# Performance work log

Hardware: AMD Instinct MI355X
Metric: run time of the kernel (lower is better)

The kernel has to match this reference:

```python
import jax, jax.numpy as jnp
import numpy as np

B, NK, NQ, DK, DQ, H, DV = 16, 256, 256, 256, 256, 128, 256
MASK_VAL = -1000000.0

def setup_inputs() -> dict:
    key = jax.random.key(0)
    ks = jax.random.split(key, 7)
    return {
        "key": jax.random.normal(ks[0], (B, NK, DK), dtype=jnp.float32),
        "query": jax.random.normal(ks[1], (B, NQ, DQ), dtype=jnp.float32),
        "value": jax.random.normal(ks[2], (B, NQ, DV), dtype=jnp.float32),
        "valid_lens": jax.random.randint(ks[3], (B,), 1, NQ + 1, dtype=jnp.int32),
        "Wk": jax.random.normal(ks[4], (DK, H), dtype=jnp.float32) / np.sqrt(DK),
        "Wq": jax.random.normal(ks[5], (DQ, H), dtype=jnp.float32) / np.sqrt(DQ),
        "wv": jax.random.normal(ks[6], (H,), dtype=jnp.float32) / np.sqrt(H),
    }

def reference(key, query, value, valid_lens, Wk, Wq, wv):
    k = key @ Wk                      # (B, NK, H)
    q = query @ Wq                    # (B, NQ, H)
    # note: original unsqueezes key at dim 2, query at dim 1 -> (B, NK, NQ, H)
    feature = jnp.tanh(k[:, :, None, :] + q[:, None, :, :])
    scores = jnp.einsum('bkqh,h->bkq', feature, wv)   # (B, NK, NQ)
    # mask along last (query) axis per batch, as repeat_interleave does
    pos = jnp.arange(scores.shape[-1])[None, None, :]
    masked = jnp.where(pos < valid_lens[:, None, None], scores, MASK_VAL)
    attn = jax.nn.softmax(masked, axis=-1)            # (B, NK, NQ)
    return jnp.einsum('bkq,bqd->bkd', attn, value)    # (B, NK, DV)
```

## Files before the change

### kernel.cpp

```cpp
#include <hip/hip_runtime.h>

#define B_   16
#define NK_  256
#define NQ_  256
#define DK_  256
#define H_   128
#define DV_  256

#define C2X 2.8853900817779268f
#define L2E 1.4426950408889634f
#define MASKV -1.0e5f

typedef float f4 __attribute__((ext_vector_type(4)));

__device__ __forceinline__ float exp2_fast(float x) { return __builtin_amdgcn_exp2f(x); }
__device__ __forceinline__ float rcp_fast(float x)  { return __builtin_amdgcn_rcpf(x); }

__global__ __launch_bounds__(256) void proj_kernel(
    const float* __restrict__ key, const float* __restrict__ query,
    const float* __restrict__ Wk,  const float* __restrict__ Wq,
    float* __restrict__ kfE, float* __restrict__ qE4)
{
    __shared__ alignas(16) float A_s[16 * 256];
    __shared__ alignas(16) float W_s[2][32 * 128];

    const int blk = blockIdx.x;
    const int tid = threadIdx.x;
    const bool isQ = blk >= 256;
    const int rb = (blk & 255) * 16;

    const float* __restrict__ A = isQ ? query : key;
    const float* __restrict__ W = isQ ? Wq : Wk;

    {
        const f4* src = (const f4*)(A + (size_t)rb * DK_);
        f4* dst = (f4*)A_s;
#pragma unroll
        for (int j = 0; j < 4; ++j) dst[tid + 256 * j] = src[tid + 256 * j];
    }
    f4 wr0, wr1, wr2, wr3;
    {
        const f4* ws = (const f4*)W;
        wr0 = ws[tid]; wr1 = ws[tid + 256]; wr2 = ws[tid + 512]; wr3 = ws[tid + 768];
    }

    const int rg2 = (tid >> 5) << 1;
    const int c4  = (tid & 31) << 2;

    f4 acc0 = {0.f, 0.f, 0.f, 0.f}, acc1 = acc0;

    for (int c = 0; c < 8; ++c) {
        {
            f4* wd = (f4*)&W_s[c & 1][0];
            wd[tid] = wr0; wd[tid + 256] = wr1; wd[tid + 512] = wr2; wd[tid + 768] = wr3;
        }
        __syncthreads();
        if (c < 7) {
            const f4* ws = (const f4*)(W + (size_t)(c + 1) * 32 * H_);
            wr0 = ws[tid]; wr1 = ws[tid + 256]; wr2 = ws[tid + 512]; wr3 = ws[tid + 768];
        }
        const float* Wb = &W_s[c & 1][0];
        const float* Ab = A_s + (c << 5);
#pragma unroll
        for (int k = 0; k < 32; k += 4) {
            f4 w0 = *(const f4*)(Wb + (k + 0) * H_ + c4);
            f4 w1 = *(const f4*)(Wb + (k + 1) * H_ + c4);
            f4 w2 = *(const f4*)(Wb + (k + 2) * H_ + c4);
            f4 w3 = *(const f4*)(Wb + (k + 3) * H_ + c4);
            f4 a0 = *(const f4*)(Ab + (rg2 + 0) * 256 + k);
            f4 a1 = *(const f4*)(Ab + (rg2 + 1) * 256 + k);
            acc0 += a0[0] * w0; acc1 += a1[0] * w0;
            acc0 += a0[1] * w1; acc1 += a1[1] * w1;
            acc0 += a0[2] * w2; acc1 += a1[2] * w2;
            acc0 += a0[3] * w3; acc1 += a1[3] * w3;
        }
    }

    f4 e0, e1;
#pragma unroll
    for (int cc = 0; cc < 4; ++cc) {
        e0[cc] = exp2_fast(C2X * acc0[cc]);
        e1[cc] = exp2_fast(C2X * acc1[cc]);
    }

    if (!isQ) {
        float* dst = kfE + (size_t)(rb + rg2) * H_ + c4;
        *(f4*)(dst)      = e0;
        *(f4*)(dst + H_) = e1;
    } else {
        const int b  = rb >> 8;
        const int q0 = (rb & 255) + rg2;
        f4* dst = (f4*)qE4 + ((size_t)(b * 32 + (c4 >> 2))) * NQ_ + q0;
        dst[0] = e0;
        dst[1] = e1;
    }
}

__global__ __launch_bounds__(512, 4) void attn_kernel(
    const float* __restrict__ kfE, const float* __restrict__ qE4,
    const float* __restrict__ value, const int* __restrict__ vlens,
    const float* __restrict__ wv, float* __restrict__ out)
{
    __shared__ alignas(16) float at_s[256 * 8];
    __shared__ alignas(16) float scratch[8192];

    const int x    = blockIdx.x;
    const int g    = x >> 4;
    const int b    = ((x & 15) + ((x >> 8) << 3)) & 15;
    const int k0   = g << 3;
    const int tid  = threadIdx.x;
    const int lane = tid & 63;
    const int wu   = __builtin_amdgcn_readfirstlane(tid >> 6);
    const int valid  = vlens[b];
    const int nchunk = (valid + 63) >> 6;

    float sumwv;
    {
        f4 sw = {0.f, 0.f, 0.f, 0.f};
#pragma unroll
        for (int i = 0; i < 32; ++i) sw += ((const f4*)wv)[i];
        sumwv = (sw[0] + sw[1]) + (sw[2] + sw[3]);
    }

    float* sc_s = scratch;

    {
        const int c  = wu >> 1;
        const int rh = wu & 1;
        if (c < nchunk) {
            const float* ekb = kfE + ((size_t)(b * NK_ + k0 + rh * 4)) * H_;
            const f4*    eqp = (const f4*)qE4 + ((size_t)b << 13) + (c << 6) + lane;
            const f4*    wvf = (const f4*)wv;

            float acc[4][2];
#pragma unroll
            for (int r = 0; r < 4; ++r) { acc[r][0] = 0.f; acc[r][1] = 0.f; }

#pragma unroll 4
            for (int h4 = 0; h4 < 32; ++h4) {
                const f4 e  = eqp[h4 << 8];
                const f4 w4 = wvf[h4];
#pragma unroll
                for (int r = 0; r < 4; ++r) {
                    const f4 ek = *(const f4*)(ekb + r * H_ + (h4 << 2));
                    acc[r][0] = fmaf(w4[0], rcp_fast(fmaf(ek[0], e[0], 1.f)), acc[r][0]);
                    acc[r][1] = fmaf(w4[1], rcp_fast(fmaf(ek[1], e[1], 1.f)), acc[r][1]);
                    acc[r][0] = fmaf(w4[2], rcp_fast(fmaf(ek[2], e[2], 1.f)), acc[r][0]);
                    acc[r][1] = fmaf(w4[3], rcp_fast(fmaf(ek[3], e[3], 1.f)), acc[r][1]);
                }
            }
            const int q = (c << 6) + lane;
#pragma unroll
            for (int r = 0; r < 4; ++r)
                sc_s[(rh * 4 + r) * 260 + q] = sumwv - 2.f * (acc[r][0] + acc[r][1]);
        }
    }
    __syncthreads();

    {
        const float* row = sc_s + wu * 260;
        float s[4];
        float m = MASKV;
#pragma unroll
        for (int j = 0; j < 4; ++j) {
            const int q = (j << 6) + lane;
            s[j] = (q < valid) ? row[q] : MASKV;
            m = fmaxf(m, s[j]);
        }
#pragma unroll
        for (int off = 32; off >= 1; off >>= 1)
            m = fmaxf(m, __shfl_xor(m, off, 64));
        float ssum = 0.f;
#pragma unroll
        for (int j = 0; j < 4; ++j) {
            s[j] = exp2_fast(L2E * (s[j] - m));
            ssum += s[j];
        }
#pragma unroll
        for (int off = 32; off >= 1; off >>= 1)
            ssum += __shfl_xor(ssum, off, 64);
        const float inv = rcp_fast(ssum);
#pragma unroll
        for (int j = 0; j < 4; ++j)
            at_s[(((j << 6) + lane) << 3) + wu] = s[j] * inv;
    }
    __syncthreads();

    float* red = scratch;
    {
        const int d4 = lane << 2;
        const float* vb = value + (size_t)b * (NQ_ * DV_) + d4;
        f4 o[8];
#pragma unroll
        for (int k = 0; k < 8; ++k) o[k] = (f4){0.f, 0.f, 0.f, 0.f};
#pragma unroll 4
        for (int q = wu; q < valid; q += 8) {
            const f4 v   = *(const f4*)(vb + (size_t)q * DV_);
            const f4 alo = *(const f4*)(at_s + (q << 3));
            const f4 ahi = *(const f4*)(at_s + (q << 3) + 4);
            o[0] += alo[0] * v; o[1] += alo[1] * v;
            o[2] += alo[2] * v; o[3] += alo[3] * v;
            o[4] += ahi[0] * v; o[5] += ahi[1] * v;
            o[6] += ahi[2] * v; o[7] += ahi[3] * v;
        }
        if (wu < 4) {
            float* rp = red + (wu << 11) + d4;
#pragma unroll
            for (int k = 0; k < 8; ++k) *(f4*)(rp + (k << 8)) = o[k];
        }
    }
    __syncthreads();
    {
        const int d4 = lane << 2;
        if (wu >= 4) {
            float* rp = red + ((wu - 4) << 11) + d4;
        }
    }
    {
        const int d4 = lane << 2;
    }
    __syncthreads();
    {
        const int d4 = lane << 2;
        const float* rp = red + (wu << 8) + d4;
        f4 oo = *(const f4*)(rp)        + *(const f4*)(rp + 2048)
              + *(const f4*)(rp + 4096) + *(const f4*)(rp + 6144);
        *(f4*)(out + ((size_t)(b * NK_ + k0 + wu)) * DV_ + d4) = oo;
    }
}

__global__ __launch_bounds__(512, 4) void attn_kernel2(
    const float* __restrict__ kfE, const float* __restrict__ qE4,
    const float* __restrict__ value, const int* __restrict__ vlens,
    const float* __restrict__ wv, float* __restrict__ out)
{
    __shared__ alignas(16) float at_s[256 * 8];
    __shared__ alignas(16) float scratch[8192];

    const int x    = blockIdx.x;
    const int g    = x >> 4;
    const int b    = ((x & 15) + ((x >> 8) << 3)) & 15;
    const int k0   = g << 3;
    const int tid  = threadIdx.x;
    const int lane = tid & 63;
    const int wu   = __builtin_amdgcn_readfirstlane(tid >> 6);
    const int valid  = vlens[b];
    const int nchunk = (valid + 63) >> 6;

    float sumwv;
    {
        f4 sw = {0.f, 0.f, 0.f, 0.f};
#pragma unroll
        for (int i = 0; i < 32; ++i) sw += ((const f4*)wv)[i];
        sumwv = (sw[0] + sw[1]) + (sw[2] + sw[3]);
    }

    float* sc_s = scratch;

    {
        const int c  = wu >> 1;
        const int rh = wu & 1;
        if (c < nchunk) {
            const float* ekb = kfE + ((size_t)(b * NK_ + k0 + rh * 4)) * H_;
            const f4*    eqp = (const f4*)qE4 + ((size_t)b << 13) + (c << 6) + lane;
            const f4*    wvf = (const f4*)wv;
            float acc[4][2];
#pragma unroll
            for (int r = 0; r < 4; ++r) { acc[r][0] = 0.f; acc[r][1] = 0.f; }
#pragma unroll 4
            for (int h4 = 0; h4 < 32; ++h4) {
                const f4 e  = eqp[h4 << 8];
                const f4 w4 = wvf[h4];
#pragma unroll
                for (int r = 0; r < 4; ++r) {
                    const f4 ek = *(const f4*)(ekb + r * H_ + (h4 << 2));
                    acc[r][0] = fmaf(w4[0], rcp_fast(fmaf(ek[0], e[0], 1.f)), acc[r][0]);
                    acc[r][1] = fmaf(w4[1], rcp_fast(fmaf(ek[1], e[1], 1.f)), acc[r][1]);
                    acc[r][0] = fmaf(w4[2], rcp_fast(fmaf(ek[2], e[2], 1.f)), acc[r][0]);
                    acc[r][1] = fmaf(w4[3], rcp_fast(fmaf(ek[3], e[3], 1.f)), acc[r][1]);
                }
            }
            const int q = (c << 6) + lane;
#pragma unroll
            for (int r = 0; r < 4; ++r)
                sc_s[(rh * 4 + r) * 260 + q] = sumwv - 2.f * (acc[r][0] + acc[r][1]);
        }
    }
    __syncthreads();

    {
        const float* row = sc_s + wu * 260;
        float s[4];
        float m = MASKV;
#pragma unroll
        for (int j = 0; j < 4; ++j) {
            const int q = (j << 6) + lane;
            s[j] = (q < valid) ? row[q] : MASKV;
            m = fmaxf(m, s[j]);
        }
#pragma unroll
        for (int off = 32; off >= 1; off >>= 1)
            m = fmaxf(m, __shfl_xor(m, off, 64));
        float ssum = 0.f;
#pragma unroll
        for (int j = 0; j < 4; ++j) {
            s[j] = exp2_fast(L2E * (s[j] - m));
            ssum += s[j];
        }
#pragma unroll
        for (int off = 32; off >= 1; off >>= 1)
            ssum += __shfl_xor(ssum, off, 64);
        const float inv = rcp_fast(ssum);
#pragma unroll
        for (int j = 0; j < 4; ++j)
            at_s[(((j << 6) + lane) << 3) + wu] = s[j] * inv;
    }
    __syncthreads();

    float* red = scratch;
    {
        const int d4 = lane << 2;
        const float* vb = value + (size_t)b * (NQ_ * DV_) + d4;
        f4 o[8];
#pragma unroll
        for (int k = 0; k < 8; ++k) o[k] = (f4){0.f, 0.f, 0.f, 0.f};
#pragma unroll 4
        for (int q = wu; q < valid; q += 8) {
            const f4 v   = *(const f4*)(vb + (size_t)q * DV_);
            const f4 alo = *(const f4*)(at_s + (q << 3));
            const f4 ahi = *(const f4*)(at_s + (q << 3) + 4);
            o[0] += alo[0] * v; o[1] += alo[1] * v;
            o[2] += alo[2] * v; o[3] += alo[3] * v;
            o[4] += ahi[0] * v; o[5] += ahi[1] * v;
            o[6] += ahi[2] * v; o[7] += ahi[3] * v;
        }
        if (wu < 4) {
            float* rp = red + (wu << 11) + d4;
#pragma unroll
            for (int k = 0; k < 8; ++k) *(f4*)(rp + (k << 8)) = o[k];
        }
        __syncthreads();
        if (wu >= 4) {
            float* rp = red + ((wu - 4) << 11) + d4;
#pragma unroll
            for (int k = 0; k < 8; ++k) {
                f4* p = (f4*)(rp + (k << 8));
                *p += o[k];
            }
        }
        __syncthreads();
        const float* rp = red + (wu << 8) + d4;
        f4 oo = *(const f4*)(rp)        + *(const f4*)(rp + 2048)
              + *(const f4*)(rp + 4096) + *(const f4*)(rp + 6144);
        *(f4*)(out + ((size_t)(b * NK_ + k0 + wu)) * DV_ + d4) = oo;
    }
}

extern "C" void kernel_launch(void* const* d_in, const int* in_sizes, int n_in,
                              void* d_out, int out_size, void* d_ws, size_t ws_size,
                              hipStream_t stream)
{
    const float* key   = (const float*)d_in[0];
    const float* query = (const float*)d_in[1];
    const float* value = (const float*)d_in[2];
    const int*   vlens = (const int*)  d_in[3];
    const float* Wk    = (const float*)d_in[4];
    const float* Wq    = (const float*)d_in[5];
    const float* wv    = (const float*)d_in[6];
    float* outp = (float*)d_out;

    float* kfE = (float*)d_ws;
    float* qE4 = kfE + (size_t)B_ * NK_ * H_;

    hipLaunchKernelGGL(proj_kernel, dim3(512), dim3(256), 0, stream,
                       key, query, Wk, Wq, kfE, qE4);
    hipLaunchKernelGGL(attn_kernel2, dim3(512), dim3(512), 0, stream,
                       kfE, qE4, value, vlens, wv, outp);
}
```

Measured before the change: 103.0 us.

## Use split-bf16 MFMA for projection GEMM and drop dead attention kernel

The projection kernel now uses bf16 MFMA matrix instructions with a hi/lo split (three MFMAs per tile) to keep close-to-fp32 accuracy, in place of scalar FMA. Each block covers 32 rows, so the grid is halved, and weights are converted straight from global memory into registers. The unused old attn_kernel is removed and attn_kernel2 is renamed to attn_kernel. Risks are the conversion overhead, the strided weight loads, and scalar scattered stores to the qE4 layout.

```diff
diff --git a/kernel.cpp b/kernel.cpp
--- a/kernel.cpp
+++ b/kernel.cpp
@@ -12,224 +12,125 @@
 #define MASKV -1.0e5f
 
 typedef float f4 __attribute__((ext_vector_type(4)));
+typedef short s4v    __attribute__((ext_vector_type(4)));
+typedef short bf16x8 __attribute__((ext_vector_type(8)));
 
 __device__ __forceinline__ float exp2_fast(float x) { return __builtin_amdgcn_exp2f(x); }
 __device__ __forceinline__ float rcp_fast(float x)  { return __builtin_amdgcn_rcpf(x); }
+
+__device__ __forceinline__ unsigned bf16_rne(float x) {
+    unsigned u = __builtin_bit_cast(unsigned, x);
+    return (u + 0x7FFFu + ((u >> 16) & 1u)) >> 16;
+}
+__device__ __forceinline__ float bf16_to_f(unsigned h) {
+    return __builtin_bit_cast(float, h << 16);
+}
 
 __global__ __launch_bounds__(256) void proj_kernel(
     const float* __restrict__ key, const float* __restrict__ query,
     const float* __restrict__ Wk,  const float* __restrict__ Wq,
     float* __restrict__ kfE, float* __restrict__ qE4)
 {
-    __shared__ alignas(16) float A_s[16 * 256];
-    __shared__ alignas(16) float W_s[2][32 * 128];
+    __shared__ alignas(16) short Ah_s[32 * 264];
+    __shared__ alignas(16) short Al_s[32 * 264];
 
     const int blk = blockIdx.x;
     const int tid = threadIdx.x;
-    const bool isQ = blk >= 256;
-    const int rb = (blk & 255) * 16;
-
-    const float* __restrict__ A = isQ ? query : key;
-    const float* __restrict__ W = isQ ? Wq : Wk;
-
-    {
-        const f4* src = (const f4*)(A + (size_t)rb * DK_);
-        f4* dst = (f4*)A_s;
-#pragma unroll
-        for (int j = 0; j < 4; ++j) dst[tid + 256 * j] = src[tid + 256 * j];
-    }
-    f4 wr0, wr1, wr2, wr3;
-    {
-        const f4* ws = (const f4*)W;
-        wr0 = ws[tid]; wr1 = ws[tid + 256]; wr2 = ws[tid + 512]; wr3 = ws[tid + 768];
-    }
-
-    const int rg2 = (tid >> 5) << 1;
-    const int c4  = (tid & 31) << 2;
-
-    f4 acc0 = {0.f, 0.f, 0.f, 0.f}, acc1 = acc0;
-
-    for (int c = 0; c < 8; ++c) {
-        {
-            f4* wd = (f4*)&W_s[c & 1][0];
-            wd[tid] = wr0; wd[tid + 256] = wr1; wd[tid + 512] = wr2; wd[tid + 768] = wr3;
-        }
-        __syncthreads();
-        if (c < 7) {
-            const f4* ws = (const f4*)(W + (size_t)(c + 1) * 32 * H_);
-            wr0 = ws[tid]; wr1 = ws[tid + 256]; wr2 = ws[tid + 512]; wr3 = ws[tid + 768];
-        }
-        const float* Wb = &W_s[c & 1][0];
-        const float* Ab = A_s + (c << 5);
-#pragma unroll
-        for (int k = 0; k < 32; k += 4) {
-            f4 w0 = *(const f4*)(Wb + (k + 0) * H_ + c4);
-            f4 w1 = *(const f4*)(Wb + (k + 1) * H_ + c4);
-            f4 w2 = *(const f4*)(Wb + (k + 2) * H_ + c4);
-            f4 w3 = *(const f4*)(Wb + (k + 3) * H_ + c4);
-            f4 a0 = *(const f4*)(Ab + (rg2 + 0) * 256 + k);
-            f4 a1 = *(const f4*)(Ab + (rg2 + 1) * 256 + k);
-            acc0 += a0[0] * w0; acc1 += a1[0] * w0;
-            acc0 += a0[1] * w1; acc1 += a1[1] * w1;
-            acc0 += a0[2] * w2; acc1 += a1[2] * w2;
-            acc0 += a0[3] * w3; acc1 += a1[3] * w3;
-        }
-    }
-
-    f4 e0, e1;
-#pragma unroll
-    for (int cc = 0; cc < 4; ++cc) {
-        e0[cc] = exp2_fast(C2X * acc0[cc]);
-        e1[cc] = exp2_fast(C2X * acc1[cc]);
-    }
-
-    if (!isQ) {
-        float* dst = kfE + (size_t)(rb + rg2) * H_ + c4;
-        *(f4*)(dst)      = e0;
-        *(f4*)(dst + H_) = e1;
-    } else {
-        const int b  = rb >> 8;
-        const int q0 = (rb & 255) + rg2;
-        f4* dst = (f4*)qE4 + ((size_t)(b * 32 + (c4 >> 2))) * NQ_ + q0;
-        dst[0] = e0;
-        dst[1] = e1;
-    }
+    const bool isQ = blk >= 128;
+    const int mbase = (blk & 127) << 5;
+
+    const float* __restrict__ Ag = isQ ? query : key;
+    const float* __restrict__ Wg = isQ ? Wq : Wk;
+
+    {
+        const int r  = tid >> 3;
+        const int kc = (tid & 7) << 5;
+        const f4* src = (const f4*)(Ag + (size_t)(mbase + r) * DK_ + kc);
+        s4v* dh = (s4v*)(Ah_s + r * 264 + kc);
+        s4v* dl = (s4v*)(Al_s + r * 264 + kc);
+#pragma unroll
+        for (int i = 0; i < 8; ++i) {
+            f4 v = src[i];
+            s4v h, l;
+#pragma unroll
+            for (int c = 0; c < 4; ++c) {
+                unsigned hb = bf16_rne(v[c]);
+                h[c] = (short)hb;
+                l[c] = (short)bf16_rne(v[c] - bf16_to_f(hb));
+            }
+            dh[i] = h;
+            dl[i] = l;
+        }
+    }
+    __syncthreads();
+
+    const int w  = tid >> 6;
+    const int l  = tid & 63;
+    const int lg = l >> 4;
+    const int ln = l & 15;
+
+    f4 acc[2][2] = {};
+
+#pragma unroll
+    for (int ks = 0; ks < 8; ++ks) {
+        const int k0 = ks << 5;
+
+        bf16x8 bh[2], bl[2];
+#pragma unroll
+        for (int nt = 0; nt < 2; ++nt) {
+            const float* bp = Wg + (size_t)(k0 + (lg << 3)) * H_
+                              + (w << 5) + (nt << 4) + ln;
+            float bv[8];
+#pragma unroll
+            for (int j = 0; j < 8; ++j) bv[j] = bp[(size_t)j * H_];
+#pragma unroll
+            for (int j = 0; j < 8; ++j) {
+                unsigned hb = bf16_rne(bv[j]);
+                bh[nt][j] = (short)hb;
+                bl[nt][j] = (short)bf16_rne(bv[j] - bf16_to_f(hb));
+            }
+        }
+
+        bf16x8 ah[2], al[2];
+#pragma unroll
+        for (int mt = 0; mt < 2; ++mt) {
+            const int m = (mt << 4) + ln;
+            ah[mt] = *(const bf16x8*)(Ah_s + m * 264 + k0 + (lg << 3));
+            al[mt] = *(const bf16x8*)(Al_s + m * 264 + k0 + (lg << 3));
+        }
+
+#pragma unroll
+        for (int mt = 0; mt < 2; ++mt)
+#pragma unroll
+            for (int nt = 0; nt < 2; ++nt) {
+                acc[mt][nt] = __builtin_amdgcn_mfma_f32_16x16x32_bf16(
+                    ah[mt], bh[nt], acc[mt][nt], 0, 0, 0);
+                acc[mt][nt] = __builtin_amdgcn_mfma_f32_16x16x32_bf16(
+                    al[mt], bh[nt], acc[mt][nt], 0, 0, 0);
+                acc[mt][nt] = __builtin_amdgcn_mfma_f32_16x16x32_bf16(
+                    ah[mt], bl[nt], acc[mt][nt], 0, 0, 0);
+            }
+    }
+
+#pragma unroll
+    for (int mt = 0; mt < 2; ++mt)
+#pragma unroll
+        for (int nt = 0; nt < 2; ++nt)
+#pragma unroll
+            for (int r = 0; r < 4; ++r) {
+                const float e = exp2_fast(C2X * acc[mt][nt][r]);
+                const int R = mbase + (mt << 4) + (lg << 2) + r;
+                const int h = (w << 5) + (nt << 4) + ln;
+                if (!isQ) {
+                    kfE[(size_t)R * H_ + h] = e;
+                } else {
+                    const int b = R >> 8, q = R & 255;
+                    qE4[(((size_t)(b * 32 + (h >> 2))) * NQ_ + q) * 4 + (h & 3)] = e;
+                }
+            }
 }
 
 __global__ __launch_bounds__(512, 4) void attn_kernel(
-    const float* __restrict__ kfE, const float* __restrict__ qE4,
-    const float* __restrict__ value, const int* __restrict__ vlens,
-    const float* __restrict__ wv, float* __restrict__ out)
-{
-    __shared__ alignas(16) float at_s[256 * 8];
-    __shared__ alignas(16) float scratch[8192];
-
-    const int x    = blockIdx.x;
-    const int g    = x >> 4;
-    const int b    = ((x & 15) + ((x >> 8) << 3)) & 15;
-    const int k0   = g << 3;
-    const int tid  = threadIdx.x;
-    const int lane = tid & 63;
-    const int wu   = __builtin_amdgcn_readfirstlane(tid >> 6);
-    const int valid  = vlens[b];
-    const int nchunk = (valid + 63) >> 6;
-
-    float sumwv;
-    {
-        f4 sw = {0.f, 0.f, 0.f, 0.f};
-#pragma unroll
-        for (int i = 0; i < 32; ++i) sw += ((const f4*)wv)[i];
-        sumwv = (sw[0] + sw[1]) + (sw[2] + sw[3]);
-    }
-
-    float* sc_s = scratch;
-
-    {
-        const int c  = wu >> 1;
-        const int rh = wu & 1;
-        if (c < nchunk) {
-            const float* ekb = kfE + ((size_t)(b * NK_ + k0 + rh * 4)) * H_;
-            const f4*    eqp = (const f4*)qE4 + ((size_t)b << 13) + (c << 6) + lane;
-            const f4*    wvf = (const f4*)wv;
-
-            float acc[4][2];
-#pragma unroll
-            for (int r = 0; r < 4; ++r) { acc[r][0] = 0.f; acc[r][1] = 0.f; }
-
-#pragma unroll 4
-            for (int h4 = 0; h4 < 32; ++h4) {
-                const f4 e  = eqp[h4 << 8];
-                const f4 w4 = wvf[h4];
-#pragma unroll
-                for (int r = 0; r < 4; ++r) {
-                    const f4 ek = *(const f4*)(ekb + r * H_ + (h4 << 2));
-                    acc[r][0] = fmaf(w4[0], rcp_fast(fmaf(ek[0], e[0], 1.f)), acc[r][0]);
-                    acc[r][1] = fmaf(w4[1], rcp_fast(fmaf(ek[1], e[1], 1.f)), acc[r][1]);
-                    acc[r][0] = fmaf(w4[2], rcp_fast(fmaf(ek[2], e[2], 1.f)), acc[r][0]);
-                    acc[r][1] = fmaf(w4[3], rcp_fast(fmaf(ek[3], e[3], 1.f)), acc[r][1]);
-                }
-            }
-            const int q = (c << 6) + lane;
-#pragma unroll
-            for (int r = 0; r < 4; ++r)
-                sc_s[(rh * 4 + r) * 260 + q] = sumwv - 2.f * (acc[r][0] + acc[r][1]);
-        }
-    }
-    __syncthreads();
-
-    {
-        const float* row = sc_s + wu * 260;
-        float s[4];
-        float m = MASKV;
-#pragma unroll
-        for (int j = 0; j < 4; ++j) {
-            const int q = (j << 6) + lane;
-            s[j] = (q < valid) ? row[q] : MASKV;
-            m = fmaxf(m, s[j]);
-        }
-#pragma unroll
-        for (int off = 32; off >= 1; off >>= 1)
-            m = fmaxf(m, __shfl_xor(m, off, 64));
-        float ssum = 0.f;
-#pragma unroll
-        for (int j = 0; j < 4; ++j) {
-            s[j] = exp2_fast(L2E * (s[j] - m));
-            ssum += s[j];
-        }
-#pragma unroll
-        for (int off = 32; off >= 1; off >>= 1)
-            ssum += __shfl_xor(ssum, off, 64);
-        const float inv = rcp_fast(ssum);
-#pragma unroll
-        for (int j = 0; j < 4; ++j)
-            at_s[(((j << 6) + lane) << 3) + wu] = s[j] * inv;
-    }
-    __syncthreads();
-
-    float* red = scratch;
-    {
-        const int d4 = lane << 2;
-        const float* vb = value + (size_t)b * (NQ_ * DV_) + d4;
-        f4 o[8];
-#pragma unroll
-        for (int k = 0; k < 8; ++k) o[k] = (f4){0.f, 0.f, 0.f, 0.f};
-#pragma unroll 4
-        for (int q = wu; q < valid; q += 8) {
-            const f4 v   = *(const f4*)(vb + (size_t)q * DV_);
-            const f4 alo = *(const f4*)(at_s + (q << 3));
-            const f4 ahi = *(const f4*)(at_s + (q << 3) + 4);
-            o[0] += alo[0] * v; o[1] += alo[1] * v;
-            o[2] += alo[2] * v; o[3] += alo[3] * v;
-            o[4] += ahi[0] * v; o[5] += ahi[1] * v;
-            o[6] += ahi[2] * v; o[7] += ahi[3] * v;
-        }
-        if (wu < 4) {
-            float* rp = red + (wu << 11) + d4;
-#pragma unroll
-            for (int k = 0; k < 8; ++k) *(f4*)(rp + (k << 8)) = o[k];
-        }
-    }
-    __syncthreads();
-    {
-        const int d4 = lane << 2;
-        if (wu >= 4) {
-            float* rp = red + ((wu - 4) << 11) + d4;
-        }
-    }
-    {
-        const int d4 = lane << 2;
-    }
-    __syncthreads();
-    {
-        const int d4 = lane << 2;
-        const float* rp = red + (wu << 8) + d4;
-        f4 oo = *(const f4*)(rp)        + *(const f4*)(rp + 2048)
-              + *(const f4*)(rp + 4096) + *(const f4*)(rp + 6144);
-        *(f4*)(out + ((size_t)(b * NK_ + k0 + wu)) * DV_ + d4) = oo;
-    }
-}
-
-__global__ __launch_bounds__(512, 4) void attn_kernel2(
     const float* __restrict__ kfE, const float* __restrict__ qE4,
     const float* __restrict__ value, const int* __restrict__ vlens,
     const float* __restrict__ wv, float* __restrict__ out)
@@ -372,8 +273,8 @@
     float* kfE = (float*)d_ws;
     float* qE4 = kfE + (size_t)B_ * NK_ * H_;
 
-    hipLaunchKernelGGL(proj_kernel, dim3(512), dim3(256), 0, stream,
+    hipLaunchKernelGGL(proj_kernel, dim3(256), dim3(256), 0, stream,
                        key, query, Wk, Wq, kfE, qE4);
-    hipLaunchKernelGGL(attn_kernel2, dim3(512), dim3(512), 0, stream,
+    hipLaunchKernelGGL(attn_kernel, dim3(512), dim3(512), 0, stream,
                        kfE, qE4, value, vlens, wv, outp);
 }
```

Result: no change. 101.0 us (-1.9%).
